# Optimization experiments

Measured on AMD Instinct MI355X. Metric: run time of the kernel, lower is better.

## Reference

```python
import jax, jax.numpy as jnp
import numpy as np


def _kb_beta(kw, osf):
    # Beatty Kaiser-Bessel shape parameter used by gpuNUFFT
    return float(np.pi * np.sqrt((kw / osf) ** 2 * (osf - 0.5) ** 2 - 0.8))


def _deapod_1d(img_dim, grid_dim, kw, beta):
    # Inverse FT of the KB kernel evaluated on the image grid (deapodization).
    u = (np.arange(img_dim) - img_dim / 2.0) / grid_dim
    z = np.sqrt((np.pi * kw * u) ** 2 - beta ** 2 + 0j)
    a = np.real(np.sin(z) / z)  # sin->sinh automatically via complex sqrt
    return a.astype(np.float32)


def setup_inputs() -> dict:
    key = jax.random.key(0)
    k0, k1, k2, k3 = jax.random.split(key, 4)
    H = 320
    C = 16
    M = 204800
    x = jax.random.normal(k0, (H, H, 2), dtype=jnp.float32)
    csm = jax.random.normal(k1, (C, H, H, 2), dtype=jnp.float32) / jnp.sqrt(float(C))
    trajectory = jax.random.uniform(k2, (2, M), dtype=jnp.float32, minval=-0.5, maxval=0.5)
    dcf = jax.random.uniform(k3, (M,), dtype=jnp.float32, minval=0.01, maxval=1.0)
    return {"x": x, "csm": csm, "trajectory": trajectory, "dcf": dcf,
            "img_dim": 320, "osf": 2, "kernel_width": 3}


def reference(x, csm, trajectory, dcf, img_dim, osf, kernel_width):
    kw = int(kernel_width)
    G = int(osf) * int(img_dim)
    beta = _kb_beta(kw, osf)
    half = kw // 2

    xc = x[..., 0] + 1j * x[..., 1]            # [H,W] complex
    cc = csm[..., 0] + 1j * csm[..., 1]        # [C,H,W] complex

    # 1) coil images + deapodization
    a1 = _deapod_1d(img_dim, G, kw, beta)
    apod = jnp.asarray(np.outer(a1, a1))       # [H,W]
    img = cc * xc[None] / apod[None]           # [C,H,W]

    # 2) zero-pad to oversampled grid, centered FFT
    pad = (G - int(img_dim)) // 2
    C = cc.shape[0]
    grid = jnp.zeros((C, G, G), dtype=img.dtype).at[:, pad:pad + int(img_dim), pad:pad + int(img_dim)].set(img)
    ksp = jnp.fft.fftshift(
        jnp.fft.fft2(jnp.fft.ifftshift(grid, axes=(-2, -1)), axes=(-2, -1)),
        axes=(-2, -1)) / G

    # 3) Kaiser-Bessel interpolation (degridding) at non-uniform points
    p = trajectory * G + G / 2.0               # [2,M] grid coords
    ctr = jnp.rint(p)

    def kb(d):
        t = 1.0 - (2.0 * d / kw) ** 2
        return jnp.where(t > 0, jnp.i0(beta * jnp.sqrt(jnp.maximum(t, 0.0))), 0.0) / kw

    acc = jnp.zeros((C, p.shape[1]), dtype=ksp.dtype)
    for oy in range(-half, half + 1):
        ny = ctr[0] + oy
        wy = kb(ny - p[0])
        iy = jnp.mod(ny, G).astype(jnp.int32)
        for ox in range(-half, half + 1):
            nx = ctr[1] + ox
            wx = kb(nx - p[1])
            ix = jnp.mod(nx, G).astype(jnp.int32)
            acc = acc + ksp[:, iy, ix] * (wy * wx)[None].astype(ksp.dtype)

    # 4) density compensation (sqrt weighting, as in optox gpuNUFFT wrapper)
    y = acc * jnp.sqrt(dcf)[None].astype(acc.dtype)
    return jnp.stack([jnp.real(y), jnp.imag(y)], axis=-1)  # [C,M,2] float32
```

## Files before the change

### kernel.cpp

```cpp
#include <hip/hip_runtime.h>
#include <hip/hip_fp16.h>

#define PI_F      3.14159265358979323846f
#define TWO_PI_F  6.28318530717958647692f
#define BETA      6.4860766f
#define NM        204800
#define NBIN      1600
#define BCAP      256
#define CPAD      16
#define HALO      18
#define HP2S      20
#define TS16      649
#define TS8       649

__device__ __forceinline__ float2 cmulf(float2 a, float2 b){
    return make_float2(a.x*b.x - a.y*b.y, a.x*b.y + a.y*b.x);
}

__device__ __forceinline__ float kbw(float d){
    float v = 1.0f - d*d*(4.0f/9.0f);
    float p = 7.983104e-6f;
    p = fmaf(p, v, 1.0930295e-4f);
    p = fmaf(p, v, 1.2575152e-3f);
    p = fmaf(p, v, 1.1956629e-2f);
    p = fmaf(p, v, 9.2085150e-2f);
    p = fmaf(p, v, 5.6035800e-1f);
    p = fmaf(p, v, 2.6107030f);
    p = fmaf(p, v, 8.9362880f);
    p = fmaf(p, v, 21.241972f);
    p = fmaf(p, v, 32.315456f);
    p = fmaf(p, v, 27.653388f);
    p = fmaf(p, v, 10.517297f);
    p = fmaf(p, v, 1.0f);
    return (v > 0.0f) ? p * (1.0f/3.0f) : 0.0f;
}

__device__ __forceinline__ int bin_of(float py, float px){
    int yy = (int)rintf(py); yy %= 640; if (yy < 0) yy += 640;
    int xx = (int)rintf(px); xx %= 640; if (xx < 0) xx += 640;
    return (yy >> 4) * 40 + (xx >> 4);
}

__global__ __launch_bounds__(1024) void k_init(float2* __restrict__ tw,
                                               float* __restrict__ ia1,
                                               int* __restrict__ counts){
    int tid = threadIdx.x;
    int g = blockIdx.x*1024 + tid;
    if (g < NBIN*CPAD) counts[g] = 0;
    if (blockIdx.x == 0){
        if (tid < 640){
            float sn, cs; sincosf((float)tid * (-TWO_PI_F/640.0f), &sn, &cs);
            tw[tid] = make_float2(cs, sn);
        }
        if (tid < 320){
            float u = (tid - 160.0f) * (1.0f/640.0f);
            float v = 3.0f * PI_F * u;
            float q = v*v - BETA*BETA;
            float a;
            if (q >= 0.0f){
                float z = sqrtf(q);
                a = (z > 1e-20f) ? (sinf(z)/z) : 1.0f;
            } else {
                float s = sqrtf(-q);
                a = (expf(s) - expf(-s)) / (2.0f*s);
            }
            ia1[tid] = 1.0f / (a * 25.298221281347036f);
        }
    }
}

__device__ __forceinline__ void fft640_wave(float2 r[10],
                                            const float2* __restrict__ tw,
                                            int a){
    const float c5r[5] = {1.0f, 0.30901699f, -0.80901699f, -0.80901699f, 0.30901699f};
    const float c5i[5] = {0.0f, -0.95105652f, -0.58778525f, 0.58778525f, 0.95105652f};
    float2 v0[5], v1[5];
    const int i0[5] = {0,2,4,6,8};
    const int i1[5] = {5,7,9,1,3};
    #pragma unroll
    for (int k2=0;k2<5;k2++){
        float ax=r[i0[0]].x, ay=r[i0[0]].y, bx=r[i1[0]].x, by=r[i1[0]].y;
        #pragma unroll
        for (int n2=1;n2<5;n2++){
            const int jj = (n2*k2)%5;
            ax += r[i0[n2]].x*c5r[jj] - r[i0[n2]].y*c5i[jj];
            ay += r[i0[n2]].x*c5i[jj] + r[i0[n2]].y*c5r[jj];
            bx += r[i1[n2]].x*c5r[jj] - r[i1[n2]].y*c5i[jj];
            by += r[i1[n2]].x*c5i[jj] + r[i1[n2]].y*c5r[jj];
        }
        v0[k2]=make_float2(ax,ay); v1[k2]=make_float2(bx,by);
    }
    float2 y[10];
    const int o0[5] = {0,6,2,8,4};
    const int o1[5] = {5,1,7,3,9};
    #pragma unroll
    for (int k2=0;k2<5;k2++){
        y[o0[k2]] = make_float2(v0[k2].x+v1[k2].x, v0[k2].y+v1[k2].y);
        y[o1[k2]] = make_float2(v0[k2].x-v1[k2].x, v0[k2].y-v1[k2].y);
    }
    float2 w1 = tw[a]; w1.x = -w1.x; w1.y = -w1.y;
    float2 w = w1;
    r[0] = y[0];
    #pragma unroll
    for (int q=1;q<10;q++){
        r[q] = cmulf(y[q], w);
        if (q < 9) w = cmulf(w, w1);
    }
    float2 ws = tw[5*a];
    #pragma unroll
    for (int h=32; h>=1; h>>=1){
        ws = cmulf(ws, ws);
        bool up = (a & h) != 0;
        if (up){ ws.x = -ws.x; ws.y = -ws.y; }
        #pragma unroll
        for (int q=0;q<10;q++){
            float px = __shfl_xor(r[q].x, h);
            float py = __shfl_xor(r[q].y, h);
            if (!up){ r[q].x += px; r[q].y += py; }
            else      r[q] = cmulf(make_float2(px - r[q].x, py - r[q].y), ws);
        }
    }
}

__global__ __launch_bounds__(1024) void k_fft1s(const float2* __restrict__ x,
                                                const float2* __restrict__ csm,
                                                const float* __restrict__ ia1,
                                                const float2* __restrict__ tw,
                                                const float* __restrict__ traj,
                                                const float* __restrict__ dcf,
                                                int* __restrict__ counts,
                                                float4* __restrict__ st,
                                                __half2* __restrict__ staged,
                                                __half2* __restrict__ bufB){
    __shared__ __half2 tile[16][TS16];
    int b = blockIdx.x;
    if (b >= 320){
        int m = (b - 320)*1024 + threadIdx.x;
        float py = traj[m]      * 640.0f + 320.0f;
        float px = traj[NM + m] * 640.0f + 320.0f;
        int bi = bin_of(py, px);
        int pos = atomicAdd(&counts[bi*CPAD], 1);
        if (pos < BCAP){
            st[bi*BCAP + pos] = make_float4(py, px, sqrtf(dcf[m]), __int_as_float(m));
        } else {
            __half2 z = __floats2half2_rn(0.0f, 0.0f);
            __half2* o = staged + (size_t)m*16;
            #pragma unroll
            for (int c=0;c<16;c++) o[c] = z;
        }
        return;
    }
    int c  = b / 20;
    int y0 = (b - c*20) * 16;
    int tid = threadIdx.x;
    int w = tid >> 6;
    int a = tid & 63;
    int y = y0 + w;
    float iay = ia1[y];
    float2 r[10];
    #pragma unroll
    for (int j=0;j<10;j++){
        int n = a + 64*j;
        float2 v = make_float2(0.0f, 0.0f);
        if (n >= 160 && n < 480){
            int xi = n - 160;
            int rr = y*320 + xi;
            float2 xv = x[rr];
            float2 cv = csm[c*102400 + rr];
            float scl = iay * ia1[xi];
            if ((y + xi) & 1) scl = -scl;
            v.x = (cv.x*xv.x - cv.y*xv.y) * scl;
            v.y = (cv.x*xv.y + cv.y*xv.x) * scl;
        }
        r[j] = v;
    }
    fft640_wave(r, tw, a);
    int kbase = 10 * (__brev((unsigned)a) >> 26);
    #pragma unroll
    for (int q=0;q<10;q++) tile[w][kbase + q] = __floats2half2_rn(r[q].x, r[q].y);
    __syncthreads();
    for (int idx = tid; idx < 16*640; idx += 1024){
        int kx = idx >> 4;
        int f  = idx & 15;
        bufB[(c*640 + kx)*320 + (y0 + f)] = tile[f][kx];
    }
}

__global__ __launch_bounds__(512) void k_fft2(const __half2* __restrict__ bufB,
                                              const float2* __restrict__ tw,
                                              __half2* __restrict__ kspH){
    __shared__ __half2 tile[8][TS8];
    int b  = blockIdx.x;
    int kx = b >> 1;
    int c0 = (b & 1) * 8;
    int tid = threadIdx.x;
    int w = tid >> 6;
    int a = tid & 63;
    const __half2* src = bufB + ((size_t)(c0 + w)*640 + kx)*320;
    float2 r[10];
    #pragma unroll
    for (int j=0;j<10;j++){
        int n = a + 64*j;
        float2 v = make_float2(0.0f, 0.0f);
        if (n >= 160 && n < 480)
            v = __half22float2(src[n - 160]);
        r[j] = v;
    }
    fft640_wave(r, tw, a);
    int kbase = 10 * (__brev((unsigned)a) >> 26);
    #pragma unroll
    for (int q=0;q<10;q++) tile[w][kbase + q] = __floats2half2_rn(r[q].x, r[q].y);
    __syncthreads();
    for (int idx = tid; idx < 8*640; idx += 512){
        int ky = idx >> 3;
        int c  = idx & 7;
        kspH[((size_t)kx*640 + ky)*16 + c0 + c] = tile[c][ky];
    }
}

__global__ __launch_bounds__(256) void k_interp3(const int* __restrict__ counts,
                                                 const float4* __restrict__ st,
                                                 const __half2* __restrict__ kspH,
                                                 __half2* __restrict__ staged){
    __shared__ __half2 hal[HALO*HALO*HP2S];
    int b = blockIdx.x;
    int ns = counts[b*CPAD];
    if (ns > BCAP) ns = BCAP;
    if (ns == 0) return;
    int s0 = b * BCAP;
    int by16 = (b / 40) * 16;
    int bx16 = (b - (b/40)*40) * 16;
    int tid = threadIdx.x;
    for (int i = tid; i < HALO*HALO*4; i += 256){
        int q  = i & 3;
        int pt = i >> 2;
        int rr = pt % HALO;
        int j  = pt / HALO;
        int gy = by16 - 1 + rr; if (gy < 0) gy += 640; if (gy >= 640) gy -= 640;
        int gx = bx16 - 1 + j;  if (gx < 0) gx += 640; if (gx >= 640) gx -= 640;
        float4 raw = ((const float4*)(kspH + ((size_t)gx*640 + gy)*16))[q];
        *(float4*)&hal[(rr*HALO + j)*HP2S + q*4] = raw;
    }
    __syncthreads();
    for (int u = tid; u < 2*ns; u += 256){
        int s = u >> 1;
        int h = u & 1;
        float4 s4 = st[s0 + s];
        float py = s4.x, px = s4.y, sc = s4.z;
        int m = __float_as_int(s4.w);
        float cy = rintf(py), cx = rintf(px);
        float wy[3], wx[3];
        int ry[3], rx[3];
        #pragma unroll
        for (int j=0;j<3;j++){
            float o = (float)(j-1);
            wy[j] = kbw(cy + o - py);
            wx[j] = kbw(cx + o - px);
            int yy = (int)cy + (j-1) - (by16 - 1);
            if (yy < 0) yy += 640; if (yy >= 640) yy -= 640;
            ry[j] = yy;
            int xx = (int)cx + (j-1) - (bx16 - 1);
            if (xx < 0) xx += 640; if (xx >= 640) xx -= 640;
            rx[j] = xx;
        }
        float2 acc[8];
        #pragma unroll
        for (int c=0;c<8;c++) acc[c] = make_float2(0.0f, 0.0f);
        #pragma unroll
        for (int jy=0;jy<3;jy++){
            #pragma unroll
            for (int jx=0;jx<3;jx++){
                float w = wy[jy]*wx[jx];
                const __half2* p = &hal[(ry[jy]*HALO + rx[jx])*HP2S + h*8];
                float4 rawA = *(const float4*)(p);
                float4 rawB = *(const float4*)(p + 4);
                const __half2* ha = (const __half2*)&rawA;
                const __half2* hb = (const __half2*)&rawB;
                #pragma unroll
                for (int q=0;q<4;q++){
                    float2 va = __half22float2(ha[q]);
                    acc[q].x = fmaf(w, va.x, acc[q].x);
                    acc[q].y = fmaf(w, va.y, acc[q].y);
                    float2 vb = __half22float2(hb[q]);
                    acc[4+q].x = fmaf(w, vb.x, acc[4+q].x);
                    acc[4+q].y = fmaf(w, vb.y, acc[4+q].y);
                }
            }
        }
        __half2* o = staged + (size_t)m*16 + h*8;
        #pragma unroll
        for (int c=0;c<8;c++)
            o[c] = __floats2half2_rn(acc[c].x*sc, acc[c].y*sc);
    }
}

__global__ __launch_bounds__(256) void k_unperm(const __half2* __restrict__ staged,
                                                float4* __restrict__ out4){
    int g = blockIdx.x*256 + threadIdx.x;
    const float4* pa = (const float4*)(staged + (size_t)(2*g)*16);
    #pragma unroll
    for (int q=0;q<4;q++){
        float4 ra = pa[q];
        float4 rb = pa[q+4];
        const __half2* ha = (const __half2*)&ra;
        const __half2* hb = (const __half2*)&rb;
        #pragma unroll
        for (int k=0;k<4;k++){
            float2 va = __half22float2(ha[k]);
            float2 vb = __half22float2(hb[k]);
            out4[(size_t)(4*q + k)*102400 + g] = make_float4(va.x, va.y, vb.x, vb.y);
        }
    }
}

extern "C" void kernel_launch(void* const* d_in, const int* in_sizes, int n_in,
                              void* d_out, int out_size, void* d_ws, size_t ws_size,
                              hipStream_t stream) {
    (void)in_sizes; (void)n_in; (void)out_size; (void)ws_size;
    const float* x    = (const float*)d_in[0];
    const float* csm  = (const float*)d_in[1];
    const float* traj = (const float*)d_in[2];
    const float* dcf  = (const float*)d_in[3];
    float* out = (float*)d_out;

    char* ws = (char*)d_ws;
    float2*  tw     = (float2*)ws;
    float*   ia1    = (float*)(ws + 8192);
    int*     counts = (int*)(ws + 16384);
    float4*  st     = (float4*)(ws + 1048576);
    __half2* kspH   = (__half2*)(ws + 8388608);
    __half2* bufB   = (__half2*)(ws + 8388608 + 26214400ull);
    __half2* staged = (__half2*)(ws + 8388608 + 26214400ull + 13107200ull);

    k_init   <<<26, 1024, 0, stream>>>(tw, ia1, counts);
    k_fft1s  <<<520, 1024, 0, stream>>>((const float2*)x, (const float2*)csm, ia1, tw,
                                        traj, dcf, counts, st, staged, bufB);
    k_fft2   <<<1280, 512, 0, stream>>>(bufB, tw, kspH);
    k_interp3<<<NBIN, 256, 0, stream>>>(counts, st, kspH, staged);
    k_unperm <<<400, 256, 0, stream>>>(staged, (float4*)out);
}
```

Before: 73.02 us.

## Drop init kernel, compute twiddles inline, split k-space by coil half

Removes the k_init kernel. Counts are now zeroed with hipMemsetAsync, the FFT twiddles are computed in registers with sincosf, and the deapodization table is rebuilt in shared memory by each FFT block. The k-space buffer is split into two coil-half planes so each k_fft2 block writes a contiguous 8-coil slab, and the interpolation halo load reads from the matching plane. The goal is to cut one launch and its dependency plus the scattered strided writes, at the price of redundant per-block transcendental work and a less contiguous halo gather.

```diff
diff --git a/kernel.cpp b/kernel.cpp
--- a/kernel.cpp
+++ b/kernel.cpp
@@ -12,6 +12,7 @@
 #define HP2S      20
 #define TS16      649
 #define TS8       649
+#define KSPHALF   3276800ull
 
 __device__ __forceinline__ float2 cmulf(float2 a, float2 b){
     return make_float2(a.x*b.x - a.y*b.y, a.x*b.y + a.y*b.x);
@@ -41,37 +42,7 @@
     return (yy >> 4) * 40 + (xx >> 4);
 }
 
-__global__ __launch_bounds__(1024) void k_init(float2* __restrict__ tw,
-                                               float* __restrict__ ia1,
-                                               int* __restrict__ counts){
-    int tid = threadIdx.x;
-    int g = blockIdx.x*1024 + tid;
-    if (g < NBIN*CPAD) counts[g] = 0;
-    if (blockIdx.x == 0){
-        if (tid < 640){
-            float sn, cs; sincosf((float)tid * (-TWO_PI_F/640.0f), &sn, &cs);
-            tw[tid] = make_float2(cs, sn);
-        }
-        if (tid < 320){
-            float u = (tid - 160.0f) * (1.0f/640.0f);
-            float v = 3.0f * PI_F * u;
-            float q = v*v - BETA*BETA;
-            float a;
-            if (q >= 0.0f){
-                float z = sqrtf(q);
-                a = (z > 1e-20f) ? (sinf(z)/z) : 1.0f;
-            } else {
-                float s = sqrtf(-q);
-                a = (expf(s) - expf(-s)) / (2.0f*s);
-            }
-            ia1[tid] = 1.0f / (a * 25.298221281347036f);
-        }
-    }
-}
-
-__device__ __forceinline__ void fft640_wave(float2 r[10],
-                                            const float2* __restrict__ tw,
-                                            int a){
+__device__ __forceinline__ void fft640_wave(float2 r[10], int a){
     const float c5r[5] = {1.0f, 0.30901699f, -0.80901699f, -0.80901699f, 0.30901699f};
     const float c5i[5] = {0.0f, -0.95105652f, -0.58778525f, 0.58778525f, 0.95105652f};
     float2 v0[5], v1[5];
@@ -98,7 +69,10 @@
         y[o0[k2]] = make_float2(v0[k2].x+v1[k2].x, v0[k2].y+v1[k2].y);
         y[o1[k2]] = make_float2(v0[k2].x-v1[k2].x, v0[k2].y-v1[k2].y);
     }
-    float2 w1 = tw[a]; w1.x = -w1.x; w1.y = -w1.y;
+    float sn, cs;
+    sincosf((float)a * (-TWO_PI_F/640.0f), &sn, &cs);
+    float2 base = make_float2(cs, sn);
+    float2 w1 = make_float2(-cs, -sn);
     float2 w = w1;
     r[0] = y[0];
     #pragma unroll
@@ -106,7 +80,8 @@
         r[q] = cmulf(y[q], w);
         if (q < 9) w = cmulf(w, w1);
     }
-    float2 ws = tw[5*a];
+    float2 b2 = cmulf(base, base);
+    float2 ws = cmulf(cmulf(b2, b2), base);
     #pragma unroll
     for (int h=32; h>=1; h>>=1){
         ws = cmulf(ws, ws);
@@ -124,8 +99,6 @@
 
 __global__ __launch_bounds__(1024) void k_fft1s(const float2* __restrict__ x,
                                                 const float2* __restrict__ csm,
-                                                const float* __restrict__ ia1,
-                                                const float2* __restrict__ tw,
                                                 const float* __restrict__ traj,
                                                 const float* __restrict__ dcf,
                                                 int* __restrict__ counts,
@@ -133,9 +106,11 @@
                                                 __half2* __restrict__ staged,
                                                 __half2* __restrict__ bufB){
     __shared__ __half2 tile[16][TS16];
+    __shared__ float ia1s[320];
     int b = blockIdx.x;
+    int tid = threadIdx.x;
     if (b >= 320){
-        int m = (b - 320)*1024 + threadIdx.x;
+        int m = (b - 320)*1024 + tid;
         float py = traj[m]      * 640.0f + 320.0f;
         float px = traj[NM + m] * 640.0f + 320.0f;
         int bi = bin_of(py, px);
@@ -150,13 +125,27 @@
         }
         return;
     }
+    if (tid < 320){
+        float u = (tid - 160.0f) * (1.0f/640.0f);
+        float v = 3.0f * PI_F * u;
+        float qq = v*v - BETA*BETA;
+        float aa;
+        if (qq >= 0.0f){
+            float z = sqrtf(qq);
+            aa = (z > 1e-20f) ? (sinf(z)/z) : 1.0f;
+        } else {
+            float s = sqrtf(-qq);
+            aa = (expf(s) - expf(-s)) / (2.0f*s);
+        }
+        ia1s[tid] = 1.0f / (aa * 25.298221281347036f);
+    }
+    __syncthreads();
     int c  = b / 20;
     int y0 = (b - c*20) * 16;
-    int tid = threadIdx.x;
     int w = tid >> 6;
     int a = tid & 63;
     int y = y0 + w;
-    float iay = ia1[y];
+    float iay = ia1s[y];
     float2 r[10];
     #pragma unroll
     for (int j=0;j<10;j++){
@@ -167,14 +156,14 @@
             int rr = y*320 + xi;
             float2 xv = x[rr];
             float2 cv = csm[c*102400 + rr];
-            float scl = iay * ia1[xi];
+            float scl = iay * ia1s[xi];
             if ((y + xi) & 1) scl = -scl;
             v.x = (cv.x*xv.x - cv.y*xv.y) * scl;
             v.y = (cv.x*xv.y + cv.y*xv.x) * scl;
         }
         r[j] = v;
     }
-    fft640_wave(r, tw, a);
+    fft640_wave(r, a);
     int kbase = 10 * (__brev((unsigned)a) >> 26);
     #pragma unroll
     for (int q=0;q<10;q++) tile[w][kbase + q] = __floats2half2_rn(r[q].x, r[q].y);
@@ -187,16 +176,15 @@
 }
 
 __global__ __launch_bounds__(512) void k_fft2(const __half2* __restrict__ bufB,
-                                              const float2* __restrict__ tw,
                                               __half2* __restrict__ kspH){
     __shared__ __half2 tile[8][TS8];
     int b  = blockIdx.x;
     int kx = b >> 1;
-    int c0 = (b & 1) * 8;
+    int hh = b & 1;
     int tid = threadIdx.x;
     int w = tid >> 6;
     int a = tid & 63;
-    const __half2* src = bufB + ((size_t)(c0 + w)*640 + kx)*320;
+    const __half2* src = bufB + ((size_t)(hh*8 + w)*640 + kx)*320;
     float2 r[10];
     #pragma unroll
     for (int j=0;j<10;j++){
@@ -206,15 +194,16 @@
             v = __half22float2(src[n - 160]);
         r[j] = v;
     }
-    fft640_wave(r, tw, a);
+    fft640_wave(r, a);
     int kbase = 10 * (__brev((unsigned)a) >> 26);
     #pragma unroll
     for (int q=0;q<10;q++) tile[w][kbase + q] = __floats2half2_rn(r[q].x, r[q].y);
     __syncthreads();
+    __half2* dst = kspH + ((size_t)hh*640 + kx)*640*8;
     for (int idx = tid; idx < 8*640; idx += 512){
         int ky = idx >> 3;
         int c  = idx & 7;
-        kspH[((size_t)kx*640 + ky)*16 + c0 + c] = tile[c][ky];
+        dst[ky*8 + c] = tile[c][ky];
     }
 }
 
@@ -238,7 +227,10 @@
         int j  = pt / HALO;
         int gy = by16 - 1 + rr; if (gy < 0) gy += 640; if (gy >= 640) gy -= 640;
         int gx = bx16 - 1 + j;  if (gx < 0) gx += 640; if (gx >= 640) gx -= 640;
-        float4 raw = ((const float4*)(kspH + ((size_t)gx*640 + gy)*16))[q];
+        int hh = q >> 1;
+        int qq = q & 1;
+        const float4* src4 = (const float4*)(kspH + (((size_t)hh*640 + gx)*640 + gy)*8);
+        float4 raw = src4[qq];
         *(float4*)&hal[(rr*HALO + j)*HP2S + q*4] = raw;
     }
     __syncthreads();
@@ -324,18 +316,16 @@
     float* out = (float*)d_out;
 
     char* ws = (char*)d_ws;
-    float2*  tw     = (float2*)ws;
-    float*   ia1    = (float*)(ws + 8192);
     int*     counts = (int*)(ws + 16384);
     float4*  st     = (float4*)(ws + 1048576);
     __half2* kspH   = (__half2*)(ws + 8388608);
     __half2* bufB   = (__half2*)(ws + 8388608 + 26214400ull);
     __half2* staged = (__half2*)(ws + 8388608 + 26214400ull + 13107200ull);
 
-    k_init   <<<26, 1024, 0, stream>>>(tw, ia1, counts);
-    k_fft1s  <<<520, 1024, 0, stream>>>((const float2*)x, (const float2*)csm, ia1, tw,
+    hipMemsetAsync(counts, 0, NBIN*CPAD*sizeof(int), stream);
+    k_fft1s  <<<520, 1024, 0, stream>>>((const float2*)x, (const float2*)csm,
                                         traj, dcf, counts, st, staged, bufB);
-    k_fft2   <<<1280, 512, 0, stream>>>(bufB, tw, kspH);
+    k_fft2   <<<1280, 512, 0, stream>>>(bufB, kspH);
     k_interp3<<<NBIN, 256, 0, stream>>>(counts, st, kspH, staged);
     k_unperm <<<400, 256, 0, stream>>>(staged, (float4*)out);
 }
```

After: 73.22 us. Within noise of the previous version (+0.3%).
